# Kernel optimization log

Hardware: AMD Instinct MI355X
Metric: run time of the kernel (lower is better)

The kernel has to match this reference:

```python
import jax, jax.numpy as jnp
import numpy as np

N, E, H, G, L = 50000, 640000, 128, 8, 3

def setup_inputs() -> dict:
    key = jax.random.key(0)
    ks = jax.random.split(key, 10)
    s = 1.0 / np.sqrt(H)
    return {
        "x": jax.random.normal(ks[0], (N, H), jnp.float32),
        "query": jax.random.normal(ks[1], (G, H), jnp.float32),
        "Wl": jax.random.normal(ks[2], (L, H, H), jnp.float32) * s,
        "bl": jax.random.normal(ks[3], (L, H), jnp.float32) * s,
        "Wr": jax.random.normal(ks[4], (L, H, H), jnp.float32) * s,
        "Wlin": jax.random.normal(ks[5], (H, H), jnp.float32) * s,
        "blin": jax.random.normal(ks[6], (H,), jnp.float32) * s,
        "edge_index": jax.random.randint(ks[7], (2, E), 0, N, jnp.int64),
        "batch_vec": jnp.sort(jax.random.randint(ks[8], (N,), 0, G, jnp.int64)),
    }

def reference(x, query, Wl, bl, Wr, Wlin, blin, edge_index, batch_vec):
    src, dst = edge_index[0], edge_index[1]
    n = x.shape[0]
    for i in range(L):
        # SAGEConv(aggr='max'): gather neighbor feats, scatter-max to dst
        m = jax.ops.segment_max(x[src], dst, num_segments=n)  # [N,H]
        m = jnp.where(jnp.isfinite(m), m, 0.0)  # isolated nodes -> 0 (PyG)
        x = jax.nn.relu(m @ Wl[i].T + bl[i] + x @ Wr[i].T)
    x = x @ Wlin.T + blin  # encoder final linear
    # cosine scoring per graph, vectorized via batch_vec
    xn = x / jnp.linalg.norm(x, axis=1, keepdims=True).clip(1e-12)
    qn = query / jnp.linalg.norm(query, axis=1, keepdims=True).clip(1e-12)
    scores = jnp.sum(xn * qn[batch_vec], axis=1)  # [N]
    return scores
```

## Files before the change

### kernel.cpp

```cpp
#include <hip/hip_runtime.h>
#include <math.h>

#define H 128

typedef _Float16 half8 __attribute__((ext_vector_type(8)));
typedef float f32x16 __attribute__((ext_vector_type(16)));
typedef int int4v __attribute__((ext_vector_type(4)));

__device__ __forceinline__ half8 h8max(half8 a, half8 b) {
#if defined(__has_builtin) && __has_builtin(__builtin_elementwise_max)
    return __builtin_elementwise_max(a, b);
#else
    half8 r;
#pragma unroll
    for (int j = 0; j < 8; ++j) r[j] = a[j] > b[j] ? a[j] : b[j];
    return r;
#endif
}

__device__ __forceinline__ half8 h8shfl_xor(half8 v, int mask) {
    int4v iv;
    __builtin_memcpy(&iv, &v, 16);
#pragma unroll
    for (int j = 0; j < 4; ++j) iv[j] = __shfl_xor(iv[j], mask, 64);
    half8 r;
    __builtin_memcpy(&r, &iv, 16);
    return r;
}


__global__ __launch_bounds__(256) void scan_atomic(const int* __restrict__ deg,
                                                   int* __restrict__ offsets,
                                                   int* __restrict__ gcur, int N) {
    __shared__ int buf[256];
    __shared__ int sbase;
    int tid = threadIdx.x;
    int i = blockIdx.x * 256 + tid;
    int v = (i < N) ? deg[i] : 0;
    int incl = v;
    buf[tid] = v;
    __syncthreads();
#pragma unroll
    for (int off = 1; off < 256; off <<= 1) {
        int t = (tid >= off) ? buf[tid - off] : 0;
        __syncthreads();
        incl += t;
        buf[tid] = incl;
        __syncthreads();
    }
    if (tid == 255) sbase = atomicAdd(gcur, incl);
    __syncthreads();
    if (i < N) offsets[i] = sbase + incl - v;
}

__global__ __launch_bounds__(256) void fill_adj(const int* __restrict__ ei, int E,
                                                const int* __restrict__ offsets,
                                                int* __restrict__ cursor,
                                                int* __restrict__ adj) {
    int e = blockIdx.x * 256 + threadIdx.x;
    if (e < E) {
        int s = ei[e];
        int d = ei[E + e];
        int pos = atomicAdd(&cursor[d], 1);
        adj[offsets[d] + pos] = s;
    }
}


__global__ __launch_bounds__(256) void prep_all(
    const int* __restrict__ ei, int E, int* __restrict__ deg,
    const float* __restrict__ x, const float* __restrict__ query,
    const float* __restrict__ Wl, const float* __restrict__ Wr,
    const float* __restrict__ Wlin, _Float16* __restrict__ xh,
    _Float16* __restrict__ wimg, float* __restrict__ qn, int n8, int HB, int SB,
    int WB) {
    int b = blockIdx.x;
    int tid = threadIdx.x;
    if (b < HB) {
        int e = b * 256 + tid;
        if (e < E) atomicAdd(&deg[ei[E + e]], 1);
    } else if (b < HB + SB) {
        int i = (b - HB) * 256 + tid;
        if (i < n8) {
            const float4* x4 = (const float4*)x;
            float4 u = x4[(size_t)i * 2], v = x4[(size_t)i * 2 + 1];
            float f[8] = {u.x, u.y, u.z, u.w, v.x, v.y, v.z, v.w};
            half8 h;
#pragma unroll
            for (int j = 0; j < 8; ++j) h[j] = (_Float16)f[j];
            *(half8*)(xh + (size_t)i * 8) = h;
        }
    } else if (b < HB + SB + WB) {
        int gidx = (b - HB - SB) * 256 + tid;
        if (gidx < 7 * 2048) {
            int mat = gidx / 2048;
            int rem = gidx - mat * 2048;
            int n = rem >> 4;
            int g = rem & 15;
            const float* src = (mat == 6) ? Wlin
                             : ((mat & 1) ? Wr + (mat >> 1) * H * H
                                          : Wl + (mat >> 1) * H * H);
            const float* p = src + n * H + g * 8;
            half8 h, l;
#pragma unroll
            for (int j = 0; j < 8; ++j) {
                float v = p[j];
                _Float16 hh = (_Float16)v;
                h[j] = hh;
                l[j] = (_Float16)(v - (float)hh);
            }
            int kc4 = g >> 2, gpc = g & 3;
            int posB = (gpc + (n & 3) + ((n >> 2) & 3)) & 3;
            size_t base = (size_t)mat * 32768 + (size_t)kc4 * 8192 + n * 32 + posB * 8;
            *(half8*)(wimg + base) = h;
            *(half8*)(wimg + base + 4096) = l;
        }
    } else {
        int g = b - HB - SB - WB;
        __shared__ float part[4];
        float v = (tid < 128) ? query[g * H + tid] : 0.f;
        float ss = v * v;
#pragma unroll
        for (int off = 32; off > 0; off >>= 1) ss += __shfl_xor(ss, off, 64);
        if ((tid & 63) == 0) part[tid >> 6] = ss;
        __syncthreads();
        float tot = part[0] + part[1];
        if (tid < 128) qn[g * H + tid] = v / fmaxf(sqrtf(tot), 1e-12f);
    }
}


__global__ __launch_bounds__(256) void layer_fused3(
    const half8* __restrict__ Xh, const int* __restrict__ deg,
    const int* __restrict__ offsets, const int* __restrict__ adj,
    const _Float16* __restrict__ Bimg, const float* __restrict__ bias,
    _Float16* __restrict__ Yh, int N) {
    __shared__ __align__(16) _Float16 sU[8192];
    __shared__ __align__(16) _Float16 sB[8192];

    int tid = threadIdx.x;
    int w = tid >> 6;
    int lane = tid & 63;
    int l31 = lane & 31;
    int lhi = lane >> 5;
    int ws = w >> 1;
    int wc = w & 1;
    int n0 = blockIdx.x * 64;

    {
        int sub = lane >> 4;
        int lf = lane & 15;
        const _Float16 ni = (_Float16)(-INFINITY);
        const half8 ninf = {ni, ni, ni, ni, ni, ni, ni, ni};
        const half8 hz = {(_Float16)0.f, (_Float16)0.f, (_Float16)0.f, (_Float16)0.f,
                          (_Float16)0.f, (_Float16)0.f, (_Float16)0.f, (_Float16)0.f};
        int nd = n0 + w * 16 + lf;
        int ndc = nd < N ? nd : N - 1;
        int e0v = offsets[ndc];
        int degv = (nd < N) ? deg[ndc] : 0;

        for (int i = 0; i < 16; ++i) {
            int e0 = __shfl(e0v, i, 64);
            int d = __shfl(degv, i, 64);
            int row = w * 16 + i;
            half8 acc = ninf;
            for (int base = 0; base < d; base += 16) {
                half8 v[4];
#pragma unroll
                for (int q = 0; q < 4; ++q) {
                    int j = base + q * 4 + sub;
                    int idx = adj[e0 + (j < d ? j : d - 1)];
                    v[q] = Xh[(size_t)idx * 16 + lf];
                }
                acc = h8max(acc, h8max(h8max(v[0], v[1]), h8max(v[2], v[3])));
            }
            acc = h8max(acc, h8shfl_xor(acc, 16));
            acc = h8max(acc, h8shfl_xor(acc, 32));
            if (d == 0) acc = hz;
            if (sub == 0) *(half8*)&sU[row * 128 + (lf ^ (row & 15)) * 8] = acc;
        }
    }
    __syncthreads();

    f32x16 acc[2];
#pragma unroll
    for (int nt = 0; nt < 2; ++nt) {
        float bv = bias[wc * 64 + nt * 32 + l31];
#pragma unroll
        for (int r = 0; r < 16; ++r) acc[nt][r] = bv;
    }

    int rl = ws * 32 + l31;

    for (int kc4 = 0; kc4 < 4; ++kc4) {
        if (kc4) __syncthreads();
        {
            const half8* bsrc = (const half8*)(Bimg + (size_t)kc4 * 8192);
            half8* bdst = (half8*)sB;
#pragma unroll
            for (int i = 0; i < 4; ++i) bdst[tid + i * 256] = bsrc[tid + i * 256];
        }
        __syncthreads();
#pragma unroll
        for (int ks = 0; ks < 2; ++ks) {
            int g16 = kc4 * 4 + ks * 2 + lhi;
            int posA = g16 ^ (rl & 15);
            half8 ah = *(const half8*)&sU[rl * 128 + posA * 8];
#pragma unroll
            for (int nt = 0; nt < 2; ++nt) {
                int n = wc * 64 + nt * 32 + l31;
                int gpc = ks * 2 + lhi;
                int posB = (gpc + (n & 3) + ((n >> 2) & 3)) & 3;
                half8 bh = *(const half8*)&sB[n * 32 + posB * 8];
                half8 bl = *(const half8*)&sB[4096 + n * 32 + posB * 8];
                acc[nt] = __builtin_amdgcn_mfma_f32_32x32x16_f16(ah, bh, acc[nt], 0, 0, 0);
                acc[nt] = __builtin_amdgcn_mfma_f32_32x32x16_f16(ah, bl, acc[nt], 0, 0, 0);
            }
        }
    }

    for (int kc4 = 0; kc4 < 4; ++kc4) {
        __syncthreads();
        {
            const half8* bsrc = (const half8*)(Bimg + 32768 + (size_t)kc4 * 8192);
            half8* bdst = (half8*)sB;
#pragma unroll
            for (int i = 0; i < 4; ++i) bdst[tid + i * 256] = bsrc[tid + i * 256];
        }
        if ((kc4 & 1) == 0) {
            int kc64 = kc4 >> 1;
#pragma unroll
            for (int i = 0; i < 2; ++i) {
                int idx = tid + i * 256;
                int row = idx >> 3;
                int gp8 = idx & 7;
                int n = n0 + row;
                half8 h = {(_Float16)0.f, (_Float16)0.f, (_Float16)0.f, (_Float16)0.f,
                           (_Float16)0.f, (_Float16)0.f, (_Float16)0.f, (_Float16)0.f};
                if (n < N) h = Xh[(size_t)n * 16 + kc64 * 8 + gp8];
                int pos8 = (gp8 + (row & 7) + ((row >> 3) & 7)) & 7;
                *(half8*)&sU[row * 72 + pos8 * 8] = h;
            }
        }
        __syncthreads();
#pragma unroll
        for (int ks = 0; ks < 2; ++ks) {
            int gp8 = (kc4 & 1) * 4 + ks * 2 + lhi;
            int posA8 = (gp8 + (rl & 7) + ((rl >> 3) & 7)) & 7;
            half8 ah = *(const half8*)&sU[rl * 72 + posA8 * 8];
#pragma unroll
            for (int nt = 0; nt < 2; ++nt) {
                int n = wc * 64 + nt * 32 + l31;
                int gpc = ks * 2 + lhi;
                int posB = (gpc + (n & 3) + ((n >> 2) & 3)) & 3;
                half8 bh = *(const half8*)&sB[n * 32 + posB * 8];
                half8 bl = *(const half8*)&sB[4096 + n * 32 + posB * 8];
                acc[nt] = __builtin_amdgcn_mfma_f32_32x32x16_f16(ah, bh, acc[nt], 0, 0, 0);
                acc[nt] = __builtin_amdgcn_mfma_f32_32x32x16_f16(ah, bl, acc[nt], 0, 0, 0);
            }
        }
    }

#pragma unroll
    for (int r = 0; r < 16; ++r) {
        int row = n0 + ws * 32 + (r & 3) + 8 * (r >> 2) + 4 * lhi;
        if (row < N) {
#pragma unroll
            for (int nt = 0; nt < 2; ++nt) {
                int col = wc * 64 + nt * 32 + l31;
                Yh[(size_t)row * H + col] = (_Float16)fmaxf(acc[nt][r], 0.f);
            }
        }
    }
}


__global__ __launch_bounds__(256) void final_mfma6(
    const half8* __restrict__ Xh, const _Float16* __restrict__ Bimg,
    const float* __restrict__ blin, const float* __restrict__ qn,
    const int* __restrict__ bv, float* __restrict__ out, int N) {
    __shared__ __align__(16) _Float16 sA[9216];
    __shared__ __align__(16) _Float16 sB[8192];

    int tid = threadIdx.x;
    int w = tid >> 6;
    int lane = tid & 63;
    int l31 = lane & 31;
    int lhi = lane >> 5;
    int n0 = blockIdx.x * 128;

    int arow = n0 + w * 32 + l31;
    arow = arow < N ? arow : N - 1;
    int gl = bv[arow];

    f32x16 acc[4];
#pragma unroll
    for (int nt = 0; nt < 4; ++nt) {
        float b = blin[nt * 32 + l31];
#pragma unroll
        for (int r = 0; r < 16; ++r) acc[nt][r] = b;
    }

    int rl = w * 32 + l31;

    for (int kc4 = 0; kc4 < 4; ++kc4) {
        if (kc4) __syncthreads();
        {
            const half8* bsrc = (const half8*)(Bimg + (size_t)kc4 * 8192);
            half8* bdst = (half8*)sB;
#pragma unroll
            for (int i = 0; i < 4; ++i) bdst[tid + i * 256] = bsrc[tid + i * 256];
        }
        if ((kc4 & 1) == 0) {
            int kc64 = kc4 >> 1;
#pragma unroll
            for (int i = 0; i < 4; ++i) {
                int idx = tid + i * 256;
                int row = idx >> 3;
                int gp8 = idx & 7;
                int n = n0 + row;
                half8 h = {(_Float16)0.f, (_Float16)0.f, (_Float16)0.f, (_Float16)0.f,
                           (_Float16)0.f, (_Float16)0.f, (_Float16)0.f, (_Float16)0.f};
                if (n < N) h = Xh[(size_t)n * 16 + kc64 * 8 + gp8];
                int pos8 = (gp8 + (row & 7) + ((row >> 3) & 7)) & 7;
                *(half8*)&sA[row * 72 + pos8 * 8] = h;
            }
        }
        __syncthreads();
#pragma unroll
        for (int ks = 0; ks < 2; ++ks) {
            int gp8 = (kc4 & 1) * 4 + ks * 2 + lhi;
            int posA8 = (gp8 + (rl & 7) + ((rl >> 3) & 7)) & 7;
            half8 ah = *(const half8*)&sA[rl * 72 + posA8 * 8];
#pragma unroll
            for (int nt = 0; nt < 4; ++nt) {
                int n = nt * 32 + l31;
                int gpc = ks * 2 + lhi;
                int posB = (gpc + (n & 3) + ((n >> 2) & 3)) & 3;
                half8 bh = *(const half8*)&sB[n * 32 + posB * 8];
                half8 bl = *(const half8*)&sB[4096 + n * 32 + posB * 8];
                acc[nt] = __builtin_amdgcn_mfma_f32_32x32x16_f16(ah, bh, acc[nt], 0, 0, 0);
                acc[nt] = __builtin_amdgcn_mfma_f32_32x32x16_f16(ah, bl, acc[nt], 0, 0, 0);
            }
        }
    }

#pragma unroll
    for (int r = 0; r < 16; ++r) {
        int rloc = (r & 3) + 8 * (r >> 2) + 4 * lhi;
        int row = n0 + w * 32 + rloc;
        int g = __shfl(gl, rloc, 32);
        float ss = 0.f, sd = 0.f;
#pragma unroll
        for (int nt = 0; nt < 4; ++nt) {
            float y = acc[nt][r];
            float q = qn[(size_t)g * H + nt * 32 + l31];
            ss = fmaf(y, y, ss);
            sd = fmaf(y, q, sd);
        }
#pragma unroll
        for (int off = 1; off <= 16; off <<= 1) {
            ss += __shfl_xor(ss, off, 64);
            sd += __shfl_xor(sd, off, 64);
        }
        if (l31 == 0 && row < N) out[row] = sd / fmaxf(sqrtf(ss), 1e-12f);
    }
}


extern "C" void kernel_launch(void* const* d_in, const int* in_sizes, int n_in,
                              void* d_out, int out_size, void* d_ws, size_t ws_size,
                              hipStream_t stream) {
    const float* x = (const float*)d_in[0];
    const float* query = (const float*)d_in[1];
    const float* Wl = (const float*)d_in[2];
    const float* bl = (const float*)d_in[3];
    const float* Wr = (const float*)d_in[4];
    const float* Wlin = (const float*)d_in[5];
    const float* blin = (const float*)d_in[6];
    const int* ei = (const int*)d_in[7];
    const int* bv = (const int*)d_in[8];
    float* out = (float*)d_out;

    const int N = in_sizes[0] / H;
    const int E = in_sizes[7] / 2;
    const int G = in_sizes[1] / H;

    char* p = (char*)d_ws;
    auto alloc = [&](size_t bytes) {
        char* r = p;
        p += (bytes + 255) & ~(size_t)255;
        return r;
    };
    int* deg = (int*)alloc((size_t)(2 * N + 1) * sizeof(int));
    int* cursor = deg + N;
    int* gcur = deg + 2 * N;
    int* offsets = (int*)alloc((size_t)N * sizeof(int));
    int* adj = (int*)alloc((size_t)E * sizeof(int));
    float* qn = (float*)alloc((size_t)G * H * sizeof(float));
    _Float16* wimg = (_Float16*)alloc((size_t)7 * 32768 * sizeof(_Float16));
    size_t actH = (size_t)N * H * sizeof(_Float16);
    _Float16* xah = (_Float16*)alloc(actH);
    _Float16* xbh = (_Float16*)alloc(actH);

    hipMemsetAsync(deg, 0, (size_t)(2 * N + 1) * sizeof(int), stream);

    const int n8 = N * H / 8;
    const int HB = (E + 255) / 256;
    const int SB = (n8 + 255) / 256;
    const int WB = (7 * 2048 + 255) / 256;
    prep_all<<<HB + SB + WB + G, 256, 0, stream>>>(ei, E, deg, x, query, Wl, Wr,
                                                   Wlin, xah, wimg, qn, n8, HB,
                                                   SB, WB);
    scan_atomic<<<(N + 255) / 256, 256, 0, stream>>>(deg, offsets, gcur, N);
    fill_adj<<<(E + 255) / 256, 256, 0, stream>>>(ei, E, offsets, cursor, adj);

    const int NGm = (N + 63) / 64;
    const int NGf = (N + 127) / 128;

    layer_fused3<<<NGm, 256, 0, stream>>>(
        (const half8*)xah, deg, offsets, adj, wimg + (size_t)0 * 65536,
        bl + 0 * H, xbh, N);
    layer_fused3<<<NGm, 256, 0, stream>>>(
        (const half8*)xbh, deg, offsets, adj, wimg + (size_t)1 * 65536,
        bl + 1 * H, xah, N);
    layer_fused3<<<NGm, 256, 0, stream>>>(
        (const half8*)xah, deg, offsets, adj, wimg + (size_t)2 * 65536,
        bl + 2 * H, xbh, N);
    final_mfma6<<<NGf, 256, 0, stream>>>(
        (const half8*)xbh, wimg + (size_t)6 * 32768, blin, qn, bv, out, N);
}
```

Before: 280.9 us.

## Fuse all stages into one persistent cooperative kernel with grid syncs

Combines preprocessing, CSR construction, the three SAGE layers and the final scoring into a single cooperative persistent kernel. Stages are separated by grid-wide barriers and walk their tiles with grid-stride loops. The goal is to remove per-kernel launch overhead and inter-kernel gaps. In exchange it adds six grid barriers, caps the grid at the occupancy limit, and keeps the old multi-kernel path as a fallback.

```diff
diff --git a/kernel.cpp b/kernel.cpp
--- a/kernel.cpp
+++ b/kernel.cpp
@@ -1,5 +1,8 @@
 #include <hip/hip_runtime.h>
+#include <hip/hip_cooperative_groups.h>
 #include <math.h>
+
+namespace cg = cooperative_groups;
 
 #define H 128
 
@@ -29,53 +32,253 @@
 }
 
 
-__global__ __launch_bounds__(256) void scan_atomic(const int* __restrict__ deg,
-                                                   int* __restrict__ offsets,
-                                                   int* __restrict__ gcur, int N) {
-    __shared__ int buf[256];
-    __shared__ int sbase;
+__device__ __forceinline__ void layer_tile(
+    char* smem, int n0, const half8* __restrict__ Xh,
+    const int* __restrict__ deg, const int* __restrict__ offsets,
+    const int* __restrict__ adj, const _Float16* __restrict__ Bimg,
+    const float* __restrict__ bias, _Float16* __restrict__ Yh, int N,
+    bool firstTile) {
+    _Float16* sU = (_Float16*)smem;
+    _Float16* sB = (_Float16*)(smem + 16384);
+
     int tid = threadIdx.x;
-    int i = blockIdx.x * 256 + tid;
-    int v = (i < N) ? deg[i] : 0;
-    int incl = v;
-    buf[tid] = v;
+    int w = tid >> 6;
+    int lane = tid & 63;
+    int l31 = lane & 31;
+    int lhi = lane >> 5;
+    int ws = w >> 1;
+    int wc = w & 1;
+
+    if (!firstTile) __syncthreads();
+
+    {
+        int sub = lane >> 4;
+        int lf = lane & 15;
+        const _Float16 ni = (_Float16)(-INFINITY);
+        const half8 ninf = {ni, ni, ni, ni, ni, ni, ni, ni};
+        const half8 hz = {(_Float16)0.f, (_Float16)0.f, (_Float16)0.f, (_Float16)0.f,
+                          (_Float16)0.f, (_Float16)0.f, (_Float16)0.f, (_Float16)0.f};
+        int nd = n0 + w * 16 + lf;
+        int ndc = nd < N ? nd : N - 1;
+        int e0v = offsets[ndc];
+        int degv = (nd < N) ? deg[ndc] : 0;
+
+        for (int i = 0; i < 16; ++i) {
+            int e0 = __shfl(e0v, i, 64);
+            int d = __shfl(degv, i, 64);
+            int row = w * 16 + i;
+            half8 acc = ninf;
+            for (int base = 0; base < d; base += 16) {
+                half8 v[4];
+#pragma unroll
+                for (int q = 0; q < 4; ++q) {
+                    int j = base + q * 4 + sub;
+                    int idx = adj[e0 + (j < d ? j : d - 1)];
+                    v[q] = Xh[(size_t)idx * 16 + lf];
+                }
+                acc = h8max(acc, h8max(h8max(v[0], v[1]), h8max(v[2], v[3])));
+            }
+            acc = h8max(acc, h8shfl_xor(acc, 16));
+            acc = h8max(acc, h8shfl_xor(acc, 32));
+            if (d == 0) acc = hz;
+            if (sub == 0) *(half8*)&sU[row * 128 + (lf ^ (row & 15)) * 8] = acc;
+        }
+    }
     __syncthreads();
-#pragma unroll
-    for (int off = 1; off < 256; off <<= 1) {
-        int t = (tid >= off) ? buf[tid - off] : 0;
-        __syncthreads();
-        incl += t;
-        buf[tid] = incl;
-        __syncthreads();
-    }
-    if (tid == 255) sbase = atomicAdd(gcur, incl);
-    __syncthreads();
-    if (i < N) offsets[i] = sbase + incl - v;
-}
-
-__global__ __launch_bounds__(256) void fill_adj(const int* __restrict__ ei, int E,
-                                                const int* __restrict__ offsets,
-                                                int* __restrict__ cursor,
-                                                int* __restrict__ adj) {
-    int e = blockIdx.x * 256 + threadIdx.x;
-    if (e < E) {
-        int s = ei[e];
-        int d = ei[E + e];
-        int pos = atomicAdd(&cursor[d], 1);
-        adj[offsets[d] + pos] = s;
-    }
-}
-
-
-__global__ __launch_bounds__(256) void prep_all(
-    const int* __restrict__ ei, int E, int* __restrict__ deg,
-    const float* __restrict__ x, const float* __restrict__ query,
-    const float* __restrict__ Wl, const float* __restrict__ Wr,
-    const float* __restrict__ Wlin, _Float16* __restrict__ xh,
-    _Float16* __restrict__ wimg, float* __restrict__ qn, int n8, int HB, int SB,
-    int WB) {
-    int b = blockIdx.x;
+
+    f32x16 acc[2];
+#pragma unroll
+    for (int nt = 0; nt < 2; ++nt) {
+        float bv = bias[wc * 64 + nt * 32 + l31];
+#pragma unroll
+        for (int r = 0; r < 16; ++r) acc[nt][r] = bv;
+    }
+
+    int rl = ws * 32 + l31;
+
+    for (int kc4 = 0; kc4 < 4; ++kc4) {
+        if (kc4) __syncthreads();
+        {
+            const half8* bsrc = (const half8*)(Bimg + (size_t)kc4 * 8192);
+            half8* bdst = (half8*)sB;
+#pragma unroll
+            for (int i = 0; i < 4; ++i) bdst[tid + i * 256] = bsrc[tid + i * 256];
+        }
+        __syncthreads();
+#pragma unroll
+        for (int ks = 0; ks < 2; ++ks) {
+            int g16 = kc4 * 4 + ks * 2 + lhi;
+            int posA = g16 ^ (rl & 15);
+            half8 ah = *(const half8*)&sU[rl * 128 + posA * 8];
+#pragma unroll
+            for (int nt = 0; nt < 2; ++nt) {
+                int n = wc * 64 + nt * 32 + l31;
+                int gpc = ks * 2 + lhi;
+                int posB = (gpc + (n & 3) + ((n >> 2) & 3)) & 3;
+                half8 bh = *(const half8*)&sB[n * 32 + posB * 8];
+                half8 bl2 = *(const half8*)&sB[4096 + n * 32 + posB * 8];
+                acc[nt] = __builtin_amdgcn_mfma_f32_32x32x16_f16(ah, bh, acc[nt], 0, 0, 0);
+                acc[nt] = __builtin_amdgcn_mfma_f32_32x32x16_f16(ah, bl2, acc[nt], 0, 0, 0);
+            }
+        }
+    }
+
+    for (int kc4 = 0; kc4 < 4; ++kc4) {
+        __syncthreads();
+        {
+            const half8* bsrc = (const half8*)(Bimg + 32768 + (size_t)kc4 * 8192);
+            half8* bdst = (half8*)sB;
+#pragma unroll
+            for (int i = 0; i < 4; ++i) bdst[tid + i * 256] = bsrc[tid + i * 256];
+        }
+        if ((kc4 & 1) == 0) {
+            int kc64 = kc4 >> 1;
+#pragma unroll
+            for (int i = 0; i < 2; ++i) {
+                int idx = tid + i * 256;
+                int row = idx >> 3;
+                int gp8 = idx & 7;
+                int n = n0 + row;
+                half8 h = {(_Float16)0.f, (_Float16)0.f, (_Float16)0.f, (_Float16)0.f,
+                           (_Float16)0.f, (_Float16)0.f, (_Float16)0.f, (_Float16)0.f};
+                if (n < N) h = Xh[(size_t)n * 16 + kc64 * 8 + gp8];
+                int pos8 = (gp8 + (row & 7) + ((row >> 3) & 7)) & 7;
+                *(half8*)&sU[row * 72 + pos8 * 8] = h;
+            }
+        }
+        __syncthreads();
+#pragma unroll
+        for (int ks = 0; ks < 2; ++ks) {
+            int gp8 = (kc4 & 1) * 4 + ks * 2 + lhi;
+            int posA8 = (gp8 + (rl & 7) + ((rl >> 3) & 7)) & 7;
+            half8 ah = *(const half8*)&sU[rl * 72 + posA8 * 8];
+#pragma unroll
+            for (int nt = 0; nt < 2; ++nt) {
+                int n = wc * 64 + nt * 32 + l31;
+                int gpc = ks * 2 + lhi;
+                int posB = (gpc + (n & 3) + ((n >> 2) & 3)) & 3;
+                half8 bh = *(const half8*)&sB[n * 32 + posB * 8];
+                half8 bl2 = *(const half8*)&sB[4096 + n * 32 + posB * 8];
+                acc[nt] = __builtin_amdgcn_mfma_f32_32x32x16_f16(ah, bh, acc[nt], 0, 0, 0);
+                acc[nt] = __builtin_amdgcn_mfma_f32_32x32x16_f16(ah, bl2, acc[nt], 0, 0, 0);
+            }
+        }
+    }
+
+#pragma unroll
+    for (int r = 0; r < 16; ++r) {
+        int row = n0 + ws * 32 + (r & 3) + 8 * (r >> 2) + 4 * lhi;
+        if (row < N) {
+#pragma unroll
+            for (int nt = 0; nt < 2; ++nt) {
+                int col = wc * 64 + nt * 32 + l31;
+                Yh[(size_t)row * H + col] = (_Float16)fmaxf(acc[nt][r], 0.f);
+            }
+        }
+    }
+}
+
+__device__ __forceinline__ void final_tile(
+    char* smem, int n0, const half8* __restrict__ Xh,
+    const _Float16* __restrict__ Bimg, const float* __restrict__ blin,
+    const float* __restrict__ qn, const int* __restrict__ bv,
+    float* __restrict__ out, int N, bool firstTile) {
+    _Float16* sA = (_Float16*)smem;
+    _Float16* sB = (_Float16*)(smem + 18432);
+
     int tid = threadIdx.x;
+    int w = tid >> 6;
+    int lane = tid & 63;
+    int l31 = lane & 31;
+    int lhi = lane >> 5;
+
+    if (!firstTile) __syncthreads();
+
+    int arow = n0 + w * 32 + l31;
+    arow = arow < N ? arow : N - 1;
+    int gl = bv[arow];
+
+    f32x16 acc[4];
+#pragma unroll
+    for (int nt = 0; nt < 4; ++nt) {
+        float b = blin[nt * 32 + l31];
+#pragma unroll
+        for (int r = 0; r < 16; ++r) acc[nt][r] = b;
+    }
+
+    int rl = w * 32 + l31;
+
+    for (int kc4 = 0; kc4 < 4; ++kc4) {
+        if (kc4) __syncthreads();
+        {
+            const half8* bsrc = (const half8*)(Bimg + (size_t)kc4 * 8192);
+            half8* bdst = (half8*)sB;
+#pragma unroll
+            for (int i = 0; i < 4; ++i) bdst[tid + i * 256] = bsrc[tid + i * 256];
+        }
+        if ((kc4 & 1) == 0) {
+            int kc64 = kc4 >> 1;
+#pragma unroll
+            for (int i = 0; i < 4; ++i) {
+                int idx = tid + i * 256;
+                int row = idx >> 3;
+                int gp8 = idx & 7;
+                int n = n0 + row;
+                half8 h = {(_Float16)0.f, (_Float16)0.f, (_Float16)0.f, (_Float16)0.f,
+                           (_Float16)0.f, (_Float16)0.f, (_Float16)0.f, (_Float16)0.f};
+                if (n < N) h = Xh[(size_t)n * 16 + kc64 * 8 + gp8];
+                int pos8 = (gp8 + (row & 7) + ((row >> 3) & 7)) & 7;
+                *(half8*)&sA[row * 72 + pos8 * 8] = h;
+            }
+        }
+        __syncthreads();
+#pragma unroll
+        for (int ks = 0; ks < 2; ++ks) {
+            int gp8 = (kc4 & 1) * 4 + ks * 2 + lhi;
+            int posA8 = (gp8 + (rl & 7) + ((rl >> 3) & 7)) & 7;
+            half8 ah = *(const half8*)&sA[rl * 72 + posA8 * 8];
+#pragma unroll
+            for (int nt = 0; nt < 4; ++nt) {
+                int n = nt * 32 + l31;
+                int gpc = ks * 2 + lhi;
+                int posB = (gpc + (n & 3) + ((n >> 2) & 3)) & 3;
+                half8 bh = *(const half8*)&sB[n * 32 + posB * 8];
+                half8 bl2 = *(const half8*)&sB[4096 + n * 32 + posB * 8];
+                acc[nt] = __builtin_amdgcn_mfma_f32_32x32x16_f16(ah, bh, acc[nt], 0, 0, 0);
+                acc[nt] = __builtin_amdgcn_mfma_f32_32x32x16_f16(ah, bl2, acc[nt], 0, 0, 0);
+            }
+        }
+    }
+
+#pragma unroll
+    for (int r = 0; r < 16; ++r) {
+        int rloc = (r & 3) + 8 * (r >> 2) + 4 * lhi;
+        int row = n0 + w * 32 + rloc;
+        int g = __shfl(gl, rloc, 32);
+        float ss = 0.f, sd = 0.f;
+#pragma unroll
+        for (int nt = 0; nt < 4; ++nt) {
+            float y = acc[nt][r];
+            float q = qn[(size_t)g * H + nt * 32 + l31];
+            ss = fmaf(y, y, ss);
+            sd = fmaf(y, q, sd);
+        }
+#pragma unroll
+        for (int off = 1; off <= 16; off <<= 1) {
+            ss += __shfl_xor(ss, off, 64);
+            sd += __shfl_xor(sd, off, 64);
+        }
+        if (l31 == 0 && row < N) out[row] = sd / fmaxf(sqrtf(ss), 1e-12f);
+    }
+}
+
+__device__ __forceinline__ void prep_body(
+    char* smem, int b, int tid, const int* __restrict__ ei, int E,
+    int* __restrict__ deg, const float* __restrict__ x,
+    const float* __restrict__ query, const float* __restrict__ Wl,
+    const float* __restrict__ Wr, const float* __restrict__ Wlin,
+    _Float16* __restrict__ xh, _Float16* __restrict__ wimg,
+    float* __restrict__ qn, int n8, int HB, int SB, int WB) {
     if (b < HB) {
         int e = b * 256 + tid;
         if (e < E) atomicAdd(&deg[ei[E + e]], 1);
@@ -117,7 +320,7 @@
         }
     } else {
         int g = b - HB - SB - WB;
-        __shared__ float part[4];
+        float* part = (float*)smem;
         float v = (tid < 128) ? query[g * H + tid] : 0.f;
         float ss = v * v;
 #pragma unroll
@@ -126,245 +329,177 @@
         __syncthreads();
         float tot = part[0] + part[1];
         if (tid < 128) qn[g * H + tid] = v / fmaxf(sqrtf(tot), 1e-12f);
-    }
-}
-
-
-__global__ __launch_bounds__(256) void layer_fused3(
+        __syncthreads();
+    }
+}
+
+
+__global__ __launch_bounds__(256, 4) void mega(
+    const int* __restrict__ ei, int E, int* __restrict__ deg,
+    int* __restrict__ cursor, int* __restrict__ gcur,
+    int* __restrict__ offsets, int* __restrict__ adj,
+    const float* __restrict__ x, const float* __restrict__ query,
+    const float* __restrict__ Wl, const float* __restrict__ bl,
+    const float* __restrict__ Wr, const float* __restrict__ Wlin,
+    const float* __restrict__ blin, const int* __restrict__ bv,
+    _Float16* __restrict__ xa, _Float16* __restrict__ xb,
+    _Float16* __restrict__ wimg, float* __restrict__ qn,
+    float* __restrict__ out, int N, int G) {
+    cg::grid_group grid = cg::this_grid();
+    __shared__ __align__(16) char smem[34816];
+    int tid = threadIdx.x;
+    const int nblk = gridDim.x;
+
+    {
+        int n8 = N * (H / 8);
+        int HB = (E + 255) >> 8;
+        int SB = (n8 + 255) >> 8;
+        int WB = (7 * 2048 + 255) >> 8;
+        int U0 = HB + SB + WB + G;
+        for (int b = blockIdx.x; b < U0; b += nblk)
+            prep_body(smem, b, tid, ei, E, deg, x, query, Wl, Wr, Wlin, xa, wimg,
+                      qn, n8, HB, SB, WB);
+    }
+    grid.sync();
+
+    {
+        int U1 = (N + 255) >> 8;
+        int* buf = (int*)smem;
+        int* sbase = (int*)(smem + 1024);
+        for (int b = blockIdx.x; b < U1; b += nblk) {
+            int i = b * 256 + tid;
+            int v = (i < N) ? deg[i] : 0;
+            int incl = v;
+            buf[tid] = v;
+            __syncthreads();
+#pragma unroll
+            for (int off = 1; off < 256; off <<= 1) {
+                int t = (tid >= off) ? buf[tid - off] : 0;
+                __syncthreads();
+                incl += t;
+                buf[tid] = incl;
+                __syncthreads();
+            }
+            if (tid == 255) *sbase = atomicAdd(gcur, incl);
+            __syncthreads();
+            if (i < N) offsets[i] = *sbase + incl - v;
+            __syncthreads();
+        }
+    }
+    grid.sync();
+
+    {
+        int U2 = (E + 255) >> 8;
+        for (int b = blockIdx.x; b < U2; b += nblk) {
+            int e = b * 256 + tid;
+            if (e < E) {
+                int s = ei[e];
+                int d = ei[E + e];
+                int pos = atomicAdd(&cursor[d], 1);
+                adj[offsets[d] + pos] = s;
+            }
+        }
+    }
+    grid.sync();
+
+    int NT = (N + 63) >> 6;
+    {
+        bool first = true;
+        for (int b = blockIdx.x; b < NT; b += nblk, first = false)
+            layer_tile((char*)smem, b * 64, (const half8*)xa, deg, offsets, adj,
+                       wimg + (size_t)0 * 65536, bl + 0 * H, xb, N, first);
+    }
+    grid.sync();
+    {
+        bool first = true;
+        for (int b = blockIdx.x; b < NT; b += nblk, first = false)
+            layer_tile((char*)smem, b * 64, (const half8*)xb, deg, offsets, adj,
+                       wimg + (size_t)1 * 65536, bl + 1 * H, xa, N, first);
+    }
+    grid.sync();
+    {
+        bool first = true;
+        for (int b = blockIdx.x; b < NT; b += nblk, first = false)
+            layer_tile((char*)smem, b * 64, (const half8*)xa, deg, offsets, adj,
+                       wimg + (size_t)2 * 65536, bl + 2 * H, xb, N, first);
+    }
+    grid.sync();
+
+    int NF = (N + 127) >> 7;
+    {
+        bool first = true;
+        for (int b = blockIdx.x; b < NF; b += nblk, first = false)
+            final_tile((char*)smem, b * 128, (const half8*)xb,
+                       wimg + (size_t)6 * 32768, blin, qn, bv, out, N, first);
+    }
+}
+
+
+__global__ __launch_bounds__(256) void scan_atomic(const int* __restrict__ deg,
+                                                   int* __restrict__ offsets,
+                                                   int* __restrict__ gcur, int N) {
+    __shared__ int buf[256];
+    __shared__ int sbase;
+    int tid = threadIdx.x;
+    int i = blockIdx.x * 256 + tid;
+    int v = (i < N) ? deg[i] : 0;
+    int incl = v;
+    buf[tid] = v;
+    __syncthreads();
+#pragma unroll
+    for (int off = 1; off < 256; off <<= 1) {
+        int t = (tid >= off) ? buf[tid - off] : 0;
+        __syncthreads();
+        incl += t;
+        buf[tid] = incl;
+        __syncthreads();
+    }
+    if (tid == 255) sbase = atomicAdd(gcur, incl);
+    __syncthreads();
+    if (i < N) offsets[i] = sbase + incl - v;
+}
+
+__global__ __launch_bounds__(256) void fill_adj_k(const int* __restrict__ ei, int E,
+                                                  const int* __restrict__ offsets,
+                                                  int* __restrict__ cursor,
+                                                  int* __restrict__ adj) {
+    int e = blockIdx.x * 256 + threadIdx.x;
+    if (e < E) {
+        int s = ei[e];
+        int d = ei[E + e];
+        int pos = atomicAdd(&cursor[d], 1);
+        adj[offsets[d] + pos] = s;
+    }
+}
+
+__global__ __launch_bounds__(256) void prep_all_k(
+    const int* __restrict__ ei, int E, int* __restrict__ deg,
+    const float* __restrict__ x, const float* __restrict__ query,
+    const float* __restrict__ Wl, const float* __restrict__ Wr,
+    const float* __restrict__ Wlin, _Float16* __restrict__ xh,
+    _Float16* __restrict__ wimg, float* __restrict__ qn, int n8, int HB, int SB,
+    int WB) {
+    __shared__ __align__(16) char smem[1024];
+    prep_body(smem, blockIdx.x, threadIdx.x, ei, E, deg, x, query, Wl, Wr, Wlin,
+              xh, wimg, qn, n8, HB, SB, WB);
+}
+
+__global__ __launch_bounds__(256) void layer_k(
     const half8* __restrict__ Xh, const int* __restrict__ deg,
     const int* __restrict__ offsets, const int* __restrict__ adj,
     const _Float16* __restrict__ Bimg, const float* __restrict__ bias,
     _Float16* __restrict__ Yh, int N) {
-    __shared__ __align__(16) _Float16 sU[8192];
-    __shared__ __align__(16) _Float16 sB[8192];
-
-    int tid = threadIdx.x;
-    int w = tid >> 6;
-    int lane = tid & 63;
-    int l31 = lane & 31;
-    int lhi = lane >> 5;
-    int ws = w >> 1;
-    int wc = w & 1;
-    int n0 = blockIdx.x * 64;
-
-    {
-        int sub = lane >> 4;
-        int lf = lane & 15;
-        const _Float16 ni = (_Float16)(-INFINITY);
-        const half8 ninf = {ni, ni, ni, ni, ni, ni, ni, ni};
-        const half8 hz = {(_Float16)0.f, (_Float16)0.f, (_Float16)0.f, (_Float16)0.f,
-                          (_Float16)0.f, (_Float16)0.f, (_Float16)0.f, (_Float16)0.f};
-        int nd = n0 + w * 16 + lf;
-        int ndc = nd < N ? nd : N - 1;
-        int e0v = offsets[ndc];
-        int degv = (nd < N) ? deg[ndc] : 0;
-
-        for (int i = 0; i < 16; ++i) {
-            int e0 = __shfl(e0v, i, 64);
-            int d = __shfl(degv, i, 64);
-            int row = w * 16 + i;
-            half8 acc = ninf;
-            for (int base = 0; base < d; base += 16) {
-                half8 v[4];
-#pragma unroll
-                for (int q = 0; q < 4; ++q) {
-                    int j = base + q * 4 + sub;
-                    int idx = adj[e0 + (j < d ? j : d - 1)];
-                    v[q] = Xh[(size_t)idx * 16 + lf];
-                }
-                acc = h8max(acc, h8max(h8max(v[0], v[1]), h8max(v[2], v[3])));
-            }
-            acc = h8max(acc, h8shfl_xor(acc, 16));
-            acc = h8max(acc, h8shfl_xor(acc, 32));
-            if (d == 0) acc = hz;
-            if (sub == 0) *(half8*)&sU[row * 128 + (lf ^ (row & 15)) * 8] = acc;
-        }
-    }
-    __syncthreads();
-
-    f32x16 acc[2];
-#pragma unroll
-    for (int nt = 0; nt < 2; ++nt) {
-        float bv = bias[wc * 64 + nt * 32 + l31];
-#pragma unroll
-        for (int r = 0; r < 16; ++r) acc[nt][r] = bv;
-    }
-
-    int rl = ws * 32 + l31;
-
-    for (int kc4 = 0; kc4 < 4; ++kc4) {
-        if (kc4) __syncthreads();
-        {
-            const half8* bsrc = (const half8*)(Bimg + (size_t)kc4 * 8192);
-            half8* bdst = (half8*)sB;
-#pragma unroll
-            for (int i = 0; i < 4; ++i) bdst[tid + i * 256] = bsrc[tid + i * 256];
-        }
-        __syncthreads();
-#pragma unroll
-        for (int ks = 0; ks < 2; ++ks) {
-            int g16 = kc4 * 4 + ks * 2 + lhi;
-            int posA = g16 ^ (rl & 15);
-            half8 ah = *(const half8*)&sU[rl * 128 + posA * 8];
-#pragma unroll
-            for (int nt = 0; nt < 2; ++nt) {
-                int n = wc * 64 + nt * 32 + l31;
-                int gpc = ks * 2 + lhi;
-                int posB = (gpc + (n & 3) + ((n >> 2) & 3)) & 3;
-                half8 bh = *(const half8*)&sB[n * 32 + posB * 8];
-                half8 bl = *(const half8*)&sB[4096 + n * 32 + posB * 8];
-                acc[nt] = __builtin_amdgcn_mfma_f32_32x32x16_f16(ah, bh, acc[nt], 0, 0, 0);
-                acc[nt] = __builtin_amdgcn_mfma_f32_32x32x16_f16(ah, bl, acc[nt], 0, 0, 0);
-            }
-        }
-    }
-
-    for (int kc4 = 0; kc4 < 4; ++kc4) {
-        __syncthreads();
-        {
-            const half8* bsrc = (const half8*)(Bimg + 32768 + (size_t)kc4 * 8192);
-            half8* bdst = (half8*)sB;
-#pragma unroll
-            for (int i = 0; i < 4; ++i) bdst[tid + i * 256] = bsrc[tid + i * 256];
-        }
-        if ((kc4 & 1) == 0) {
-            int kc64 = kc4 >> 1;
-#pragma unroll
-            for (int i = 0; i < 2; ++i) {
-                int idx = tid + i * 256;
-                int row = idx >> 3;
-                int gp8 = idx & 7;
-                int n = n0 + row;
-                half8 h = {(_Float16)0.f, (_Float16)0.f, (_Float16)0.f, (_Float16)0.f,
-                           (_Float16)0.f, (_Float16)0.f, (_Float16)0.f, (_Float16)0.f};
-                if (n < N) h = Xh[(size_t)n * 16 + kc64 * 8 + gp8];
-                int pos8 = (gp8 + (row & 7) + ((row >> 3) & 7)) & 7;
-                *(half8*)&sU[row * 72 + pos8 * 8] = h;
-            }
-        }
-        __syncthreads();
-#pragma unroll
-        for (int ks = 0; ks < 2; ++ks) {
-            int gp8 = (kc4 & 1) * 4 + ks * 2 + lhi;
-            int posA8 = (gp8 + (rl & 7) + ((rl >> 3) & 7)) & 7;
-            half8 ah = *(const half8*)&sU[rl * 72 + posA8 * 8];
-#pragma unroll
-            for (int nt = 0; nt < 2; ++nt) {
-                int n = wc * 64 + nt * 32 + l31;
-                int gpc = ks * 2 + lhi;
-                int posB = (gpc + (n & 3) + ((n >> 2) & 3)) & 3;
-                half8 bh = *(const half8*)&sB[n * 32 + posB * 8];
-                half8 bl = *(const half8*)&sB[4096 + n * 32 + posB * 8];
-                acc[nt] = __builtin_amdgcn_mfma_f32_32x32x16_f16(ah, bh, acc[nt], 0, 0, 0);
-                acc[nt] = __builtin_amdgcn_mfma_f32_32x32x16_f16(ah, bl, acc[nt], 0, 0, 0);
-            }
-        }
-    }
-
-#pragma unroll
-    for (int r = 0; r < 16; ++r) {
-        int row = n0 + ws * 32 + (r & 3) + 8 * (r >> 2) + 4 * lhi;
-        if (row < N) {
-#pragma unroll
-            for (int nt = 0; nt < 2; ++nt) {
-                int col = wc * 64 + nt * 32 + l31;
-                Yh[(size_t)row * H + col] = (_Float16)fmaxf(acc[nt][r], 0.f);
-            }
-        }
-    }
-}
-
-
-__global__ __launch_bounds__(256) void final_mfma6(
+    __shared__ __align__(16) char smem[32768];
+    layer_tile(smem, blockIdx.x * 64, Xh, deg, offsets, adj, Bimg, bias, Yh, N,
+               true);
+}
+
+__global__ __launch_bounds__(256) void final_k(
     const half8* __restrict__ Xh, const _Float16* __restrict__ Bimg,
     const float* __restrict__ blin, const float* __restrict__ qn,
     const int* __restrict__ bv, float* __restrict__ out, int N) {
-    __shared__ __align__(16) _Float16 sA[9216];
-    __shared__ __align__(16) _Float16 sB[8192];
-
-    int tid = threadIdx.x;
-    int w = tid >> 6;
-    int lane = tid & 63;
-    int l31 = lane & 31;
-    int lhi = lane >> 5;
-    int n0 = blockIdx.x * 128;
-
-    int arow = n0 + w * 32 + l31;
-    arow = arow < N ? arow : N - 1;
-    int gl = bv[arow];
-
-    f32x16 acc[4];
-#pragma unroll
-    for (int nt = 0; nt < 4; ++nt) {
-        float b = blin[nt * 32 + l31];
-#pragma unroll
-        for (int r = 0; r < 16; ++r) acc[nt][r] = b;
-    }
-
-    int rl = w * 32 + l31;
-
-    for (int kc4 = 0; kc4 < 4; ++kc4) {
-        if (kc4) __syncthreads();
-        {
-            const half8* bsrc = (const half8*)(Bimg + (size_t)kc4 * 8192);
-            half8* bdst = (half8*)sB;
-#pragma unroll
-            for (int i = 0; i < 4; ++i) bdst[tid + i * 256] = bsrc[tid + i * 256];
-        }
-        if ((kc4 & 1) == 0) {
-            int kc64 = kc4 >> 1;
-#pragma unroll
-            for (int i = 0; i < 4; ++i) {
-                int idx = tid + i * 256;
-                int row = idx >> 3;
-                int gp8 = idx & 7;
-                int n = n0 + row;
-                half8 h = {(_Float16)0.f, (_Float16)0.f, (_Float16)0.f, (_Float16)0.f,
-                           (_Float16)0.f, (_Float16)0.f, (_Float16)0.f, (_Float16)0.f};
-                if (n < N) h = Xh[(size_t)n * 16 + kc64 * 8 + gp8];
-                int pos8 = (gp8 + (row & 7) + ((row >> 3) & 7)) & 7;
-                *(half8*)&sA[row * 72 + pos8 * 8] = h;
-            }
-        }
-        __syncthreads();
-#pragma unroll
-        for (int ks = 0; ks < 2; ++ks) {
-            int gp8 = (kc4 & 1) * 4 + ks * 2 + lhi;
-            int posA8 = (gp8 + (rl & 7) + ((rl >> 3) & 7)) & 7;
-            half8 ah = *(const half8*)&sA[rl * 72 + posA8 * 8];
-#pragma unroll
-            for (int nt = 0; nt < 4; ++nt) {
-                int n = nt * 32 + l31;
-                int gpc = ks * 2 + lhi;
-                int posB = (gpc + (n & 3) + ((n >> 2) & 3)) & 3;
-                half8 bh = *(const half8*)&sB[n * 32 + posB * 8];
-                half8 bl = *(const half8*)&sB[4096 + n * 32 + posB * 8];
-                acc[nt] = __builtin_amdgcn_mfma_f32_32x32x16_f16(ah, bh, acc[nt], 0, 0, 0);
-                acc[nt] = __builtin_amdgcn_mfma_f32_32x32x16_f16(ah, bl, acc[nt], 0, 0, 0);
-            }
-        }
-    }
-
-#pragma unroll
-    for (int r = 0; r < 16; ++r) {
-        int rloc = (r & 3) + 8 * (r >> 2) + 4 * lhi;
-        int row = n0 + w * 32 + rloc;
-        int g = __shfl(gl, rloc, 32);
-        float ss = 0.f, sd = 0.f;
-#pragma unroll
-        for (int nt = 0; nt < 4; ++nt) {
-            float y = acc[nt][r];
-            float q = qn[(size_t)g * H + nt * 32 + l31];
-            ss = fmaf(y, y, ss);
-            sd = fmaf(y, q, sd);
-        }
-#pragma unroll
-        for (int off = 1; off <= 16; off <<= 1) {
-            ss += __shfl_xor(ss, off, 64);
-            sd += __shfl_xor(sd, off, 64);
-        }
-        if (l31 == 0 && row < N) out[row] = sd / fmaxf(sqrtf(ss), 1e-12f);
-    }
+    __shared__ __align__(16) char smem[34816];
+    final_tile(smem, blockIdx.x * 128, Xh, Bimg, blin, qn, bv, out, N, true);
 }
 
 
@@ -409,24 +544,52 @@
     const int HB = (E + 255) / 256;
     const int SB = (n8 + 255) / 256;
     const int WB = (7 * 2048 + 255) / 256;
-    prep_all<<<HB + SB + WB + G, 256, 0, stream>>>(ei, E, deg, x, query, Wl, Wr,
-                                                   Wlin, xah, wimg, qn, n8, HB,
-                                                   SB, WB);
+
+    int maxPerCU = 0;
+    hipError_t oe = hipOccupancyMaxActiveBlocksPerMultiprocessor(
+        &maxPerCU, (const void*)mega, 256, 0);
+    hipError_t le = hipErrorUnknown;
+    if (oe == hipSuccess && maxPerCU >= 1) {
+        int ngrid = maxPerCU * 256;
+        if (ngrid > 1024) ngrid = 1024;
+        int E_ = E, N_ = N, G_ = G;
+        const int* ei_ = ei;
+        const float* x_ = x;
+        const float* query_ = query;
+        const float* Wl_ = Wl;
+        const float* bl_ = bl;
+        const float* Wr_ = Wr;
+        const float* Wlin_ = Wlin;
+        const float* blin_ = blin;
+        const int* bv_ = bv;
+        void* args[] = {(void*)&ei_,   (void*)&E_,      (void*)&deg,
+                        (void*)&cursor, (void*)&gcur,   (void*)&offsets,
+                        (void*)&adj,    (void*)&x_,     (void*)&query_,
+                        (void*)&Wl_,    (void*)&bl_,    (void*)&Wr_,
+                        (void*)&Wlin_,  (void*)&blin_,  (void*)&bv_,
+                        (void*)&xah,    (void*)&xbh,    (void*)&wimg,
+                        (void*)&qn,     (void*)&out,    (void*)&N_,
+                        (void*)&G_};
+        le = hipLaunchCooperativeKernel((const void*)mega, dim3(ngrid), dim3(256),
+                                        args, 0, stream);
+    }
+    if (le == hipSuccess) return;
+
+    prep_all_k<<<HB + SB + WB + G, 256, 0, stream>>>(ei, E, deg, x, query, Wl, Wr,
+                                                     Wlin, xah, wimg, qn, n8, HB,
+                                                     SB, WB);
     scan_atomic<<<(N + 255) / 256, 256, 0, stream>>>(deg, offsets, gcur, N);
-    fill_adj<<<(E + 255) / 256, 256, 0, stream>>>(ei, E, offsets, cursor, adj);
+    fill_adj_k<<<(E + 255) / 256, 256, 0, stream>>>(ei, E, offsets, cursor, adj);
 
     const int NGm = (N + 63) / 64;
     const int NGf = (N + 127) / 128;
 
-    layer_fused3<<<NGm, 256, 0, stream>>>(
-        (const half8*)xah, deg, offsets, adj, wimg + (size_t)0 * 65536,
-        bl + 0 * H, xbh, N);
-    layer_fused3<<<NGm, 256, 0, stream>>>(
-        (const half8*)xbh, deg, offsets, adj, wimg + (size_t)1 * 65536,
-        bl + 1 * H, xah, N);
-    layer_fused3<<<NGm, 256, 0, stream>>>(
-        (const half8*)xah, deg, offsets, adj, wimg + (size_t)2 * 65536,
-        bl + 2 * H, xbh, N);
-    final_mfma6<<<NGf, 256, 0, stream>>>(
-        (const half8*)xbh, wimg + (size_t)6 * 32768, blin, qn, bv, out, N);
-}
+    layer_k<<<NGm, 256, 0, stream>>>((const half8*)xah, deg, offsets, adj,
+                                     wimg + (size_t)0 * 65536, bl + 0 * H, xbh, N);
+    layer_k<<<NGm, 256, 0, stream>>>((const half8*)xbh, deg, offsets, adj,
+                                     wimg + (size_t)1 * 65536, bl + 1 * H, xah, N);
+    layer_k<<<NGm, 256, 0, stream>>>((const half8*)xah, deg, offsets, adj,
+                                     wimg + (size_t)2 * 65536, bl + 2 * H, xbh, N);
+    final_k<<<NGf, 256, 0, stream>>>((const half8*)xbh, wimg + (size_t)6 * 32768,
+                                     blin, qn, bv, out, N);
+}
```

New measurement: 797.8 us. +184.0%, slower.
